# Optimization experiments

Measured on AMD Instinct MI355X. Metric: run time of the kernel, lower is better.

Reference implementation:

```python
import jax, jax.numpy as jnp
import numpy as np

B, T, HID = 4, 4096, 768
H, D = 12, 64
N_HASHES = 2
BUCKET_SIZE = T // 32          # reformer repo config: max_seq_len // 32 = 128
N_BUCKETS = T // BUCKET_SIZE   # 32
SELF_ATTN_VALUE = -5e4         # reformer_pytorch TOKEN_SELF_ATTN_VALUE
MASK_VALUE = -1e9


def lsh_attention(X, mask_bool, W_qk, W_v, rotations):
    # X: [b, t, hid]; rotations: [d, n_hashes, n_buckets//2] (shared across batch & heads)
    b, t, _ = X.shape
    d, n_hashes, half_nb = rotations.shape
    n_buckets = 2 * half_nb
    h = W_qk.shape[0] // d
    scale = d ** -0.5

    qk = X @ W_qk.T            # shared query/key projection (bias-free in reformer_pytorch)
    v = X @ W_v.T

    def merge_heads(x):  # [b,t,h*d] -> [b*h, t, d]
        return x.reshape(b, t, h, d).transpose(0, 2, 1, 3).reshape(b * h, t, d)

    qk, v = merge_heads(qk), merge_heads(v)
    maskbh = jnp.repeat(mask_bool, h, axis=0)          # [bh, t]

    # --- LSH bucketing ---
    rotated = jnp.einsum('btf,fhi->bhti', qk, rotations)          # [bh, nh, t, nb/2]
    rotated = jnp.concatenate([rotated, -rotated], axis=-1)       # [bh, nh, t, nb]
    buckets = jnp.argmax(rotated, axis=-1)                        # [bh, nh, t]
    offsets = (jnp.arange(n_hashes) * n_buckets)[None, :, None]
    buckets = (buckets + offsets).reshape(b * h, n_hashes * t)

    # --- stable sort by (bucket, position) ---
    total = n_hashes * t
    ticker = jnp.arange(total)[None, :]
    buckets_and_t = buckets * t + (ticker % t)
    sticker = jnp.argsort(buckets_and_t, axis=-1)   # stable
    undo = jnp.argsort(sticker, axis=-1)
    st = sticker % t                                 # original positions, sorted order

    sqk = jnp.take_along_axis(qk, st[..., None], axis=1)
    sv = jnp.take_along_axis(v, st[..., None], axis=1)
    smask = jnp.take_along_axis(maskbh, st, axis=1)

    # --- chunk; each chunk attends to itself + previous chunk ---
    n_chunks = n_hashes * n_buckets
    cl = total // n_chunks                                  # == bucket_size
    bq_t = st.reshape(b * h, n_chunks, cl)
    bqk = sqk.reshape(b * h, n_chunks, cl, d)
    bv = sv.reshape(b * h, n_chunks, cl, d)
    bmask = smask.reshape(b * h, n_chunks, cl)

    bq = bqk
    bk = bqk / jnp.clip(jnp.linalg.norm(bqk, axis=-1, keepdims=True), 1e-12)

    def look_one_back(x):
        return jnp.concatenate([x, jnp.roll(x, 1, axis=1)], axis=2)

    bk, bv = look_one_back(bk), look_one_back(bv)
    bkv_t = look_one_back(bq_t)
    bkv_mask = look_one_back(bmask)

    dots = jnp.einsum('bnie,bnje->bnij', bq, bk) * scale    # [bh, n_chunks, cl, 2cl]
    pad = bmask[..., :, None] & bkv_mask[..., None, :]
    dots = jnp.where(pad, dots, MASK_VALUE)
    self_mask = bq_t[..., :, None] == bkv_t[..., None, :]
    dots = jnp.where(self_mask, SELF_ATTN_VALUE, dots)

    lse = jax.scipy.special.logsumexp(dots, axis=-1, keepdims=True)
    probs = jnp.exp(dots - lse)
    bo = jnp.einsum('bnij,bnje->bnie', probs, bv)

    # --- unsort and combine hash rounds via softmax over round logsumexps ---
    so = bo.reshape(b * h, total, d)
    slogits = lse.reshape(b * h, total)
    o = jnp.take_along_axis(so, undo[..., None], axis=1)
    logits = jnp.take_along_axis(slogits, undo, axis=1)

    o = o.reshape(b * h, n_hashes, t, d)
    logits = logits.reshape(b * h, n_hashes, t, 1)
    round_probs = jnp.exp(logits - jax.scipy.special.logsumexp(logits, axis=1, keepdims=True))
    out = jnp.sum(o * round_probs, axis=1)                  # [bh, t, d]
    return out.reshape(b, h, t, d).transpose(0, 2, 1, 3).reshape(b, t, h * d)


def setup_inputs() -> dict:
    key = jax.random.key(0)
    ks = jax.random.split(key, 8)
    s = 1.0 / np.sqrt(HID)
    return {
        'X': jax.random.normal(ks[0], (B, T, HID), jnp.float32),
        'mask': jnp.ones((B, T), jnp.float32),
        'W_qk': jax.random.uniform(ks[1], (H * D, HID), jnp.float32, -s, s),
        'W_v': jax.random.uniform(ks[2], (H * D, HID), jnp.float32, -s, s),
        'rotations': jax.random.normal(ks[3], (D, N_HASHES, N_BUCKETS // 2), jnp.float32),
        'W_to': jax.random.uniform(ks[4], (HID, H * D), jnp.float32, -s, s),
        'b_to': jnp.zeros((HID,), jnp.float32),
        'W_o': jax.random.uniform(ks[5], (HID, HID), jnp.float32, -s, s),
        'b_o': jnp.zeros((HID,), jnp.float32),
    }


def reference(X, mask, W_qk, W_v, rotations, W_to, b_to, W_o, b_o):
    attn = lsh_attention(X, mask.astype(bool), W_qk, W_v, rotations)
    attn = attn @ W_to.T + b_to     # LSHSelfAttention.to_out
    return attn @ W_o.T + b_o       # ReformerAttention.W_o
```

## Files before the change

### kernel.cpp

```cpp
#include <hip/hip_runtime.h>
#include <hip/hip_bf16.h>
#include <math.h>


typedef __attribute__((ext_vector_type(8))) short bf16x8;
typedef __attribute__((ext_vector_type(4))) float f32x4;

__device__ __forceinline__ float bf_lo(unsigned int w) { return __uint_as_float(w << 16); }
__device__ __forceinline__ float bf_hi(unsigned int w) { return __uint_as_float(w & 0xffff0000u); }
__device__ __forceinline__ float load_in(const void* p, size_t i, bool f32) {
  return f32 ? ((const float*)p)[i]
             : __bfloat162float(((const __hip_bfloat16*)p)[i]);
}
__device__ __forceinline__ unsigned short f2bf(float x) {
  __hip_bfloat16 h = __float2bfloat16(x);
  return *reinterpret_cast<unsigned short*>(&h);
}
__device__ __forceinline__ float bf2f(unsigned short u) { return __uint_as_float(((unsigned int)u) << 16); }

__global__ void k_detect(const unsigned int* __restrict__ X, int* __restrict__ flag) {
  if (threadIdx.x == 0 && blockIdx.x == 0) {
    int vote = 0;
    for (int i = 0; i < 64; ++i) {
      unsigned int e = (X[i] >> 7) & 0xffu;
      vote += (e >= 100u && e <= 141u) ? 1 : 0;
    }
    *flag = (vote < 32) ? 1 : 0;
  }
}

__global__ __launch_bounds__(256) void k_convert(
    const void* __restrict__ src, unsigned short* __restrict__ dst, int n,
    const int* __restrict__ flag) {
  const bool f32in = (*flag != 0);
  int i = blockIdx.x * 256 + threadIdx.x;
  if (i >= n) return;
  if (f32in) dst[i] = f2bf(((const float*)src)[i]);
  else       dst[i] = ((const unsigned short*)src)[i];
}

__global__ __launch_bounds__(256) void k_build_wrot(
    const void* __restrict__ Wqk, const void* __restrict__ rot,
    double* __restrict__ WrotT, const int* __restrict__ flag) {
  const bool f32in = (*flag != 0);
  int idx = blockIdx.x * 256 + threadIdx.x;
  if (idx >= 768 * 384) return;
  int row = idx % 384;
  int c   = idx / 384;
  int hh = row >> 5, hi = row & 31;
  double s = 0.0;
  for (int f = 0; f < 64; ++f) {
    double rv = (double)load_in(rot, f * 32 + hi, f32in);
    double wv = (double)load_in(Wqk, (size_t)(hh * 64 + f) * 768 + c, f32in);
    s = fma(rv, wv, s);
  }
  WrotT[(size_t)c * 384 + row] = s;
}

__global__ __launch_bounds__(256) void k_bucket(
    const void* __restrict__ X, const double* __restrict__ WrotT,
    unsigned char* __restrict__ cls, const int* __restrict__ flag) {
  const bool f32in = (*flag != 0);
  __shared__ double SH[6336];
  double* Xs = SH;
  double* Ws = SH + 2080;
  double* Sc = SH;
  const int tid = threadIdx.x;
  const int M0 = blockIdx.x * 128;
  const int N0 = blockIdx.y * 96;
  const int tm = tid >> 4, tn = tid & 15;
  const int sr = tid >> 1, sh = tid & 1;
  const int wk = tid >> 4, wg = tid & 15;

  double acc[8][6];
  #pragma unroll
  for (int i = 0; i < 8; ++i)
    #pragma unroll
    for (int j = 0; j < 6; ++j) acc[i][j] = 0.0;

  for (int k0 = 0; k0 < 768; k0 += 16) {
    __syncthreads();
    {
      size_t base = (size_t)(M0 + sr) * 768 + k0 + sh * 8;
      double xv[8];
      if (f32in) {
        const float4* fp = (const float4*)((const float*)X + base);
        float4 f0 = fp[0], f1 = fp[1];
        xv[0] = f0.x; xv[1] = f0.y; xv[2] = f0.z; xv[3] = f0.w;
        xv[4] = f1.x; xv[5] = f1.y; xv[6] = f1.z; xv[7] = f1.w;
      } else {
        uint4 u = *(const uint4*)((const unsigned short*)X + base);
        xv[0] = (double)bf_lo(u.x); xv[1] = (double)bf_hi(u.x);
        xv[2] = (double)bf_lo(u.y); xv[3] = (double)bf_hi(u.y);
        xv[4] = (double)bf_lo(u.z); xv[5] = (double)bf_hi(u.z);
        xv[6] = (double)bf_lo(u.w); xv[7] = (double)bf_hi(u.w);
      }
      #pragma unroll
      for (int j = 0; j < 8; ++j) Xs[(sh * 8 + j) * 130 + sr] = xv[j];
    }
    {
      const double* wp = WrotT + (size_t)(k0 + wk) * 384 + N0 + wg * 6;
      #pragma unroll
      for (int e = 0; e < 6; ++e) Ws[wk * 98 + wg * 6 + e] = wp[e];
    }
    __syncthreads();
    #pragma unroll
    for (int k = 0; k < 16; ++k) {
      double a_[8], b_[6];
      #pragma unroll
      for (int i = 0; i < 8; ++i) a_[i] = Xs[k * 130 + tm * 8 + i];
      #pragma unroll
      for (int j = 0; j < 6; ++j) b_[j] = Ws[k * 98 + tn * 6 + j];
      #pragma unroll
      for (int i = 0; i < 8; ++i)
        #pragma unroll
        for (int j = 0; j < 6; ++j)
          acc[i][j] = fma(a_[i], b_[j], acc[i][j]);
    }
  }

  #pragma unroll
  for (int chunk = 0; chunk < 2; ++chunk) {
    __syncthreads();
    if ((tm >> 3) == chunk) {
      #pragma unroll
      for (int tt = 0; tt < 8; ++tt)
        #pragma unroll
        for (int rr = 0; rr < 6; ++rr)
          Sc[(tn * 6 + rr) * 66 + (tm & 7) * 8 + tt] = acc[tt][rr];
    }
    __syncthreads();
    for (int task = tid; task < 384; task += 256) {
      int g = task >> 6, tok = task & 63;
      const double* s = &Sc[(g * 16) * 66 + tok];
      double mx = -1.0e300;
      #pragma unroll
      for (int i = 0; i < 16; ++i) {
        double a = s[i * 66];
        mx = fmax(mx, fmax(a, -a));
      }
      int amax = 0;
      #pragma unroll
      for (int i = 15; i >= 0; --i) if (-s[i * 66] == mx) amax = 16 + i;
      #pragma unroll
      for (int i = 15; i >= 0; --i) if (s[i * 66] == mx) amax = i;
      int m = M0 + chunk * 64 + tok;
      int b = m >> 12, t = m & 4095;
      int gg = blockIdx.y * 6 + g, hh = gg >> 1, h = gg & 1;
      cls[(size_t)(b * 12 + hh) * 8192 + h * 4096 + t] = (unsigned char)(h * 32 + amax);
    }
  }
}

__global__ __launch_bounds__(1024) void k_sort(
    const unsigned char* __restrict__ clsg,
    unsigned short* __restrict__ stick) {
  __shared__ unsigned short cntg[128 * 64];
  __shared__ int classbase[64];
  const int row = blockIdx.x;
  const int tid = threadIdx.x;
  const int wave = tid >> 6, lane = tid & 63;
  const unsigned char* cr = clsg + ((size_t)row << 13);

  for (int i = tid; i < 128 * 64 / 2; i += 1024) ((uint32_t*)cntg)[i] = 0;
  __syncthreads();

  unsigned char myc[8], myrank[8];
  const unsigned long long ltmask = (lane == 0) ? 0ull : (~0ull >> (64 - lane));
  #pragma unroll
  for (int chunk = 0; chunk < 8; ++chunk) {
    int g = chunk * 16 + wave;
    int j = g * 64 + lane;
    int c = cr[j];
    unsigned long long same = ~0ull;
    #pragma unroll
    for (int bit = 0; bit < 6; ++bit) {
      unsigned long long bm = __ballot((c >> bit) & 1);
      same &= ((c >> bit) & 1) ? bm : ~bm;
    }
    int rank = __popcll(same & ltmask);
    if (rank == 0) cntg[g * 64 + c] = (unsigned short)__popcll(same);
    myc[chunk] = (unsigned char)c;
    myrank[chunk] = (unsigned char)rank;
  }
  __syncthreads();
  if (tid < 64) {
    int run = 0;
    for (int g = 0; g < 128; ++g) {
      int t = cntg[g * 64 + tid];
      cntg[g * 64 + tid] = (unsigned short)run;
      run += t;
    }
    classbase[tid] = run;
  }
  __syncthreads();
  if (tid == 0) {
    int run = 0;
    for (int c = 0; c < 64; ++c) { int t = classbase[c]; classbase[c] = run; run += t; }
  }
  __syncthreads();
  unsigned short* out = stick + ((size_t)row << 13);
  #pragma unroll
  for (int chunk = 0; chunk < 8; ++chunk) {
    int g = chunk * 16 + wave;
    int j = g * 64 + lane;
    int c = myc[chunk];
    int pos = classbase[c] + cntg[g * 64 + c] + myrank[chunk];
    out[pos] = (unsigned short)j;
  }
}

__global__ __launch_bounds__(256) void k_gemm_mfma(
    const unsigned short* __restrict__ A, const unsigned short* __restrict__ W,
    const void* __restrict__ bias, void* __restrict__ Cout,
    int layout, int out_ext, const int* __restrict__ flag) {
  const bool f32in = (*flag != 0);
  const bool oF32 = out_ext && f32in;
  __shared__ unsigned short As[128 * 40];
  __shared__ unsigned short Bs[128 * 40];
  const int tid = threadIdx.x;
  const int bm = blockIdx.x, bn = blockIdx.y;
  const int w = tid >> 6, lane = tid & 63;
  const int l15 = lane & 15, lq = lane >> 4;
  const int wm = (w >> 1) * 64, wn = (w & 1) * 64;
  const int r4 = tid >> 2, c4 = tid & 3;
  const unsigned short* Ag = A + (size_t)(bm * 128 + r4) * 768 + c4 * 8;
  const unsigned short* Bg = W + (size_t)(bn * 128 + r4) * 768 + c4 * 8;
  f32x4 acc[4][4];
  #pragma unroll
  for (int i = 0; i < 4; ++i)
    #pragma unroll
    for (int j = 0; j < 4; ++j) acc[i][j] = (f32x4){0.f, 0.f, 0.f, 0.f};
  uint4 pa0 = *(const uint4*)(Ag);
  uint4 pa1 = *(const uint4*)(Ag + 64 * 768);
  uint4 pb0 = *(const uint4*)(Bg);
  uint4 pb1 = *(const uint4*)(Bg + 64 * 768);
  for (int kt = 0; kt < 24; ++kt) {
    __syncthreads();
    *(uint4*)&As[r4 * 40 + c4 * 8] = pa0;
    *(uint4*)&As[(r4 + 64) * 40 + c4 * 8] = pa1;
    *(uint4*)&Bs[r4 * 40 + c4 * 8] = pb0;
    *(uint4*)&Bs[(r4 + 64) * 40 + c4 * 8] = pb1;
    __syncthreads();
    if (kt < 23) {
      int off = (kt + 1) * 32;
      pa0 = *(const uint4*)(Ag + off);
      pa1 = *(const uint4*)(Ag + 64 * 768 + off);
      pb0 = *(const uint4*)(Bg + off);
      pb1 = *(const uint4*)(Bg + 64 * 768 + off);
    }
    bf16x8 af[4], bfr[4];
    #pragma unroll
    for (int mt = 0; mt < 4; ++mt)
      af[mt] = *(const bf16x8*)&As[(wm + mt * 16 + l15) * 40 + lq * 8];
    #pragma unroll
    for (int nt = 0; nt < 4; ++nt)
      bfr[nt] = *(const bf16x8*)&Bs[(wn + nt * 16 + l15) * 40 + lq * 8];
    #pragma unroll
    for (int mt = 0; mt < 4; ++mt)
      #pragma unroll
      for (int nt = 0; nt < 4; ++nt)
        acc[mt][nt] = __builtin_amdgcn_mfma_f32_16x16x32_bf16(af[mt], bfr[nt], acc[mt][nt], 0, 0, 0);
  }
  #pragma unroll
  for (int mt = 0; mt < 4; ++mt) {
    #pragma unroll
    for (int nt = 0; nt < 4; ++nt) {
      #pragma unroll
      for (int reg = 0; reg < 4; ++reg) {
        int m = bm * 128 + wm + mt * 16 + lq * 4 + reg;
        int n = bn * 128 + wn + nt * 16 + l15;
        float val = acc[mt][nt][reg];
        if (bias != nullptr) val += load_in(bias, n, f32in);
        if (layout == 0) {
          size_t addr = (size_t)m * 768 + n;
          if (oF32) ((float*)Cout)[addr] = val;
          else      ((unsigned short*)Cout)[addr] = f2bf(val);
        } else {
          int b2 = m >> 12, t2 = m & 4095, hh = n >> 6, f = n & 63;
          ((unsigned short*)Cout)[((((size_t)(b2 * 12 + hh)) << 12) + t2) * 64 + f] = f2bf(val);
        }
      }
    }
  }
}

__global__ __launch_bounds__(256) void k_norm(
    const unsigned short* __restrict__ qk, float* __restrict__ nk) {
  int row = blockIdx.x * 32 + (threadIdx.x >> 3);
  int cs = threadIdx.x & 7;
  const uint4* p = (const uint4*)(qk + (size_t)row * 64);
  uint4 wv = p[cs];
  float s = 0.f;
  float e;
  e = bf_lo(wv.x); s += e * e;  e = bf_hi(wv.x); s += e * e;
  e = bf_lo(wv.y); s += e * e;  e = bf_hi(wv.y); s += e * e;
  e = bf_lo(wv.z); s += e * e;  e = bf_hi(wv.z); s += e * e;
  e = bf_lo(wv.w); s += e * e;  e = bf_hi(wv.w); s += e * e;
  s += __shfl_xor(s, 1, 64);
  s += __shfl_xor(s, 2, 64);
  s += __shfl_xor(s, 4, 64);
  if (cs == 0) nk[row] = 1.0f / fmaxf(sqrtf(s), 1e-12f);
}

__global__ __launch_bounds__(256) void k_attn_mfma(
    const unsigned short* __restrict__ qk,
    const unsigned short* __restrict__ vv,
    const unsigned short* __restrict__ stick,
    const void* __restrict__ mask,
    const float* __restrict__ nk,
    unsigned short* __restrict__ o_r,
    float* __restrict__ lse_r,
    const int* __restrict__ flag) {
  const bool f32in = (*flag != 0);
  __shared__ unsigned short Qs[128 * 72];
  __shared__ unsigned short Ks[64 * 72];
  __shared__ unsigned short Vt[64 * 72];
  __shared__ unsigned short Ps[4 * 32 * 72];
  __shared__ unsigned short Tq[128];
  __shared__ unsigned short Tkv[64];
  __shared__ float Nkv[64];
  unsigned short* Vs = Ps;

  const int tid = threadIdx.x;
  const int bh = blockIdx.x >> 6;
  const int ci = blockIdx.x & 63;
  const int b  = bh / 12;
  const int prev = (ci + 63) & 63;
  const int w = tid >> 6, lane = tid & 63;
  const int l15 = lane & 15, lq = lane >> 4;
  const unsigned short* srow = stick + ((size_t)bh << 13);
  const int jrow = tid >> 3, cs = tid & 7;

  #pragma unroll
  for (int pass = 0; pass < 4; ++pass) {
    int r = jrow + pass * 32;
    int s = srow[ci * 128 + r];
    int t = s & 4095;
    uint4 qw = ((const uint4*)(qk + ((((size_t)bh << 12) + t) << 6)))[cs];
    *(uint4*)&Qs[r * 72 + cs * 8] = qw;
    if (cs == 0) {
      float mv = load_in(mask, b * 4096 + t, f32in);
      Tq[r] = (unsigned short)(s | ((mv != 0.0f) ? 0 : 0x8000));
    }
  }
  __syncthreads();

  unsigned short tqr[2][4];
  #pragma unroll
  for (int mt = 0; mt < 2; ++mt)
    #pragma unroll
    for (int reg = 0; reg < 4; ++reg)
      tqr[mt][reg] = Tq[w * 32 + mt * 16 + lq * 4 + reg];

  float m_run[2][4], l_run[2][4];
  f32x4 oacc[2][4];
  #pragma unroll
  for (int mt = 0; mt < 2; ++mt)
    #pragma unroll
    for (int reg = 0; reg < 4; ++reg) { m_run[mt][reg] = -3.0e38f; l_run[mt][reg] = 0.0f; }
  #pragma unroll
  for (int mt = 0; mt < 2; ++mt)
    #pragma unroll
    for (int nto = 0; nto < 4; ++nto) oacc[mt][nto] = (f32x4){0.f, 0.f, 0.f, 0.f};

  for (int kt = 0; kt < 4; ++kt) {
    __syncthreads();
    #pragma unroll
    for (int pass = 0; pass < 2; ++pass) {
      int j = jrow + pass * 32;
      int chunk = (kt < 2) ? ci : prev;
      int s = srow[chunk * 128 + (kt & 1) * 64 + j];
      int t = s & 4095;
      const uint4* kb = (const uint4*)(qk + ((((size_t)bh << 12) + t) << 6));
      *(uint4*)&Ks[j * 72 + cs * 8] = kb[cs];
      const uint4* vb = (const uint4*)(vv + ((((size_t)bh << 12) + t) << 6));
      int sw = (cs ^ (j & 7) ^ (j >> 3)) & 7;
      *(uint4*)&Vs[j * 72 + sw * 8] = vb[cs];
      if (cs == 0) {
        float mv = load_in(mask, b * 4096 + t, f32in);
        Tkv[j] = (unsigned short)(t | ((mv != 0.0f) ? 0 : 0x8000));
        Nkv[j] = nk[((size_t)bh << 12) + t] * 0.125f;
      }
    }
    __syncthreads();

    #pragma unroll
    for (int i = 0; i < 8; ++i) {
      int cp = w * 8 + i;
      int q8 = cp >> 2;
      int sw = (q8 ^ (lane & 7) ^ (lane >> 3)) & 7;
      uint32_t wv = *(const uint32_t*)&Vs[lane * 72 + sw * 8 + ((2 * cp) & 7)];
      Vt[(2 * cp) * 72 + lane]     = (unsigned short)(wv & 0xffff);
      Vt[(2 * cp + 1) * 72 + lane] = (unsigned short)(wv >> 16);
    }

    f32x4 sacc[2][4];
    #pragma unroll
    for (int mt = 0; mt < 2; ++mt)
      #pragma unroll
      for (int nt = 0; nt < 4; ++nt) sacc[mt][nt] = (f32x4){0.f, 0.f, 0.f, 0.f};
    #pragma unroll
    for (int ks = 0; ks < 2; ++ks) {
      bf16x8 af[2];
      #pragma unroll
      for (int mt = 0; mt < 2; ++mt)
        af[mt] = *(const bf16x8*)&Qs[(w * 32 + mt * 16 + l15) * 72 + ks * 32 + lq * 8];
      #pragma unroll
      for (int nt = 0; nt < 4; ++nt) {
        bf16x8 bfr = *(const bf16x8*)&Ks[(nt * 16 + l15) * 72 + ks * 32 + lq * 8];
        #pragma unroll
        for (int mt = 0; mt < 2; ++mt)
          sacc[mt][nt] = __builtin_amdgcn_mfma_f32_16x16x32_bf16(af[mt], bfr, sacc[mt][nt], 0, 0, 0);
      }
    }

    unsigned short tkc[4];
    float nkc[4];
    #pragma unroll
    for (int nt = 0; nt < 4; ++nt) {
      tkc[nt] = Tkv[nt * 16 + l15];
      nkc[nt] = Nkv[nt * 16 + l15];
    }
    float dv[2][4][4];
    #pragma unroll
    for (int mt = 0; mt < 2; ++mt)
      #pragma unroll
      for (int nt = 0; nt < 4; ++nt)
        #pragma unroll
        for (int reg = 0; reg < 4; ++reg) {
          float x = sacc[mt][nt][reg] * nkc[nt];
          unsigned short ts = tqr[mt][reg];
          if (((tkc[nt] | ts) & 0x8000) != 0) x = -1.0e9f;
          if (((tkc[nt] ^ ts) & 0x0fff) == 0) x = -5.0e4f;
          dv[mt][nt][reg] = x;
        }
    float mn[2][4], scv[2][4];
    #pragma unroll
    for (int mt = 0; mt < 2; ++mt)
      #pragma unroll
      for (int reg = 0; reg < 4; ++reg) {
        float rm = fmaxf(fmaxf(dv[mt][0][reg], dv[mt][1][reg]),
                         fmaxf(dv[mt][2][reg], dv[mt][3][reg]));
        rm = fmaxf(rm, __shfl_xor(rm, 1, 64));
        rm = fmaxf(rm, __shfl_xor(rm, 2, 64));
        rm = fmaxf(rm, __shfl_xor(rm, 4, 64));
        rm = fmaxf(rm, __shfl_xor(rm, 8, 64));
        float mnew = fmaxf(m_run[mt][reg], rm);
        scv[mt][reg] = __expf(m_run[mt][reg] - mnew);
        m_run[mt][reg] = mnew;
        mn[mt][reg] = mnew;
      }
    #pragma unroll
    for (int mt = 0; mt < 2; ++mt)
      #pragma unroll
      for (int nt = 0; nt < 4; ++nt)
        #pragma unroll
        for (int reg = 0; reg < 4; ++reg)
          dv[mt][nt][reg] = __expf(dv[mt][nt][reg] - mn[mt][reg]);
    #pragma unroll
    for (int mt = 0; mt < 2; ++mt)
      #pragma unroll
      for (int reg = 0; reg < 4; ++reg) {
        float rs = ((dv[mt][0][reg] + dv[mt][1][reg]) + (dv[mt][2][reg] + dv[mt][3][reg]));
        rs += __shfl_xor(rs, 1, 64);
        rs += __shfl_xor(rs, 2, 64);
        rs += __shfl_xor(rs, 4, 64);
        rs += __shfl_xor(rs, 8, 64);
        l_run[mt][reg] = l_run[mt][reg] * scv[mt][reg] + rs;
      }
    #pragma unroll
    for (int mt = 0; mt < 2; ++mt)
      #pragma unroll
      for (int nto = 0; nto < 4; ++nto)
        #pragma unroll
        for (int reg = 0; reg < 4; ++reg)
          oacc[mt][nto][reg] *= scv[mt][reg];

    __syncthreads();

    #pragma unroll
    for (int mt = 0; mt < 2; ++mt)
      #pragma unroll
      for (int nt = 0; nt < 4; ++nt)
        #pragma unroll
        for (int reg = 0; reg < 4; ++reg)
          Ps[w * 2304 + (mt * 16 + lq * 4 + reg) * 72 + nt * 16 + l15] = f2bf(dv[mt][nt][reg]);

    #pragma unroll
    for (int ks = 0; ks < 2; ++ks) {
      bf16x8 pf[2];
      #pragma unroll
      for (int mt = 0; mt < 2; ++mt)
        pf[mt] = *(const bf16x8*)&Ps[w * 2304 + (mt * 16 + l15) * 72 + ks * 32 + lq * 8];
      #pragma unroll
      for (int nto = 0; nto < 4; ++nto) {
        bf16x8 vf = *(const bf16x8*)&Vt[(nto * 16 + l15) * 72 + ks * 32 + lq * 8];
        #pragma unroll
        for (int mt = 0; mt < 2; ++mt)
          oacc[mt][nto] = __builtin_amdgcn_mfma_f32_16x16x32_bf16(pf[mt], vf, oacc[mt][nto], 0, 0, 0);
      }
    }
  }

  float invl[2][4];
  #pragma unroll
  for (int mt = 0; mt < 2; ++mt)
    #pragma unroll
    for (int reg = 0; reg < 4; ++reg) {
      float lr = l_run[mt][reg];
      invl[mt][reg] = 1.0f / lr;
      if (l15 == 0) {
        int Rr = w * 32 + mt * 16 + lq * 4 + reg;
        int s = Tq[Rr];
        int tq0 = s & 4095, rq0 = (s >> 12) & 1;
        lse_r[(((size_t)(bh * 2 + rq0)) << 12) + tq0] = m_run[mt][reg] + __logf(lr);
      }
    }
  #pragma unroll
  for (int mt = 0; mt < 2; ++mt)
    #pragma unroll
    for (int nto = 0; nto < 4; ++nto)
      #pragma unroll
      for (int reg = 0; reg < 4; ++reg)
        Ps[w * 2304 + (mt * 16 + lq * 4 + reg) * 72 + nto * 16 + l15] =
            f2bf(oacc[mt][nto][reg] * invl[mt][reg]);
  #pragma unroll
  for (int pass = 0; pass < 4; ++pass) {
    int rl = pass * 8 + (lane >> 3);
    int s = Tq[w * 32 + rl];
    int tq0 = s & 4095, rq0 = (s >> 12) & 1;
    uint4 ov = *(const uint4*)&Ps[w * 2304 + rl * 72 + (lane & 7) * 8];
    *(uint4*)(o_r + ((((size_t)(bh * 2 + rq0)) << 12) + tq0) * 64 + (lane & 7) * 8) = ov;
  }
}

__global__ __launch_bounds__(256) void k_combine(
    const unsigned short* __restrict__ o_r,
    const float* __restrict__ lse_r,
    unsigned short* __restrict__ attn) {
  int idx = blockIdx.x * 256 + threadIdx.x;
  if (idx >= 48 * 4096 * 64) return;
  int f = idx & 63;
  int t = (idx >> 6) & 4095;
  int bh = idx >> 18;
  float l0 = lse_r[((size_t)(bh * 2 + 0) << 12) + t];
  float l1 = lse_r[((size_t)(bh * 2 + 1) << 12) + t];
  float mm = fmaxf(l0, l1);
  float e0 = __expf(l0 - mm), e1 = __expf(l1 - mm);
  float inv = 1.0f / (e0 + e1);
  float o0 = bf2f(o_r[(((size_t)(bh * 2 + 0) << 12) + t) * 64 + f]);
  float o1 = bf2f(o_r[(((size_t)(bh * 2 + 1) << 12) + t) * 64 + f]);
  float res = (e0 * o0 + e1 * o1) * inv;
  int b = bh / 12, hh = bh % 12;
  attn[((size_t)(b * 4096 + t)) * 768 + hh * 64 + f] = f2bf(res);
}

extern "C" void kernel_launch(void* const* d_in, const int* in_sizes, int n_in,
                              void* d_out, int out_size, void* d_ws, size_t ws_size,
                              hipStream_t stream) {
  (void)in_sizes; (void)n_in; (void)out_size; (void)ws_size;
  const void* X    = d_in[0];
  const void* mask = d_in[1];
  const void* Wqk  = d_in[2];
  const void* Wv   = d_in[3];
  const void* rot  = d_in[4];
  const void* Wto  = d_in[5];
  const void* bto  = d_in[6];
  const void* Wo   = d_in[7];
  const void* bo   = d_in[8];

  char* ws = (char*)d_ws;
  int*            flag  = (int*)(ws);
  unsigned short* stick = (unsigned short*)(ws + 256);
  float*          lse_r = (float*)(ws + 786688);
  float*          nk    = (float*)(ws + 2359552);
  unsigned short* qk    = (unsigned short*)(ws + 3145984);
  unsigned short* v     = (unsigned short*)(ws + 28311808);
  unsigned short* o_r   = (unsigned short*)(ws + 53477632);
  double*         WrotT = (double*)(ws + 53477632);
  unsigned char*  cls   = (unsigned char*)(ws + 55836928);
  unsigned short* Wqkb  = (unsigned short*)(ws + 56230144);
  unsigned short* Wvb   = (unsigned short*)(ws + 57409792);
  unsigned short* Xb    = (unsigned short*)(ws + 58589440);
  unsigned short* Wtob  = (unsigned short*)(ws + 53477632);
  unsigned short* Wob   = (unsigned short*)(ws + 54657280);
  unsigned short* attn  = v;
  unsigned short* tmp   = qk;

  k_detect<<<1, 64, 0, stream>>>((const unsigned int*)X, flag);
  k_convert<<<49152, 256, 0, stream>>>(X, Xb, 12582912, flag);
  k_convert<<<2304, 256, 0, stream>>>(Wqk, Wqkb, 589824, flag);
  k_convert<<<2304, 256, 0, stream>>>(Wv, Wvb, 589824, flag);
  k_build_wrot<<<1152, 256, 0, stream>>>(Wqk, rot, WrotT, flag);
  k_bucket<<<dim3(128, 4), 256, 0, stream>>>(X, WrotT, cls, flag);
  k_sort<<<48, 1024, 0, stream>>>(cls, stick);
  k_gemm_mfma<<<dim3(128, 6), 256, 0, stream>>>(Xb, Wqkb, nullptr, qk, 1, 0, flag);
  k_gemm_mfma<<<dim3(128, 6), 256, 0, stream>>>(Xb, Wvb,  nullptr, v,  1, 0, flag);
  k_norm<<<6144, 256, 0, stream>>>(qk, nk);
  k_attn_mfma<<<3072, 256, 0, stream>>>(qk, v, stick, mask, nk, o_r, lse_r, flag);
  k_combine<<<49152, 256, 0, stream>>>(o_r, lse_r, attn);
  k_convert<<<2304, 256, 0, stream>>>(Wto, Wtob, 589824, flag);
  k_convert<<<2304, 256, 0, stream>>>(Wo, Wob, 589824, flag);
  k_gemm_mfma<<<dim3(128, 6), 256, 0, stream>>>(attn, Wtob, bto, tmp, 0, 0, flag);
  k_gemm_mfma<<<dim3(128, 6), 256, 0, stream>>>(tmp, Wob, bo, d_out, 0, 1, flag);
}
```

Measured before the change: 696.9 us.

## Prefetch bucket GEMM tiles in registers and fuse key-norm into attention

The fp64 bucketing GEMM now uses a K-tile of 32 instead of 16. The next X and WrotT tile is loaded into registers while the current tile is being computed, and the kernel gets a launch_bounds occupancy hint of 2. Separately, the standalone k_norm launch is removed and each key's inverse L2 norm is computed inside the attention kernel from the K row it already loads, using a shuffle reduction. This trades one launch and its global round trip for recomputing norms per chunk, at the cost of extra shared memory and register pressure in k_bucket.

```diff
diff --git a/kernel.cpp b/kernel.cpp
--- a/kernel.cpp
+++ b/kernel.cpp
@@ -57,20 +57,20 @@
   WrotT[(size_t)c * 384 + row] = s;
 }
 
-__global__ __launch_bounds__(256) void k_bucket(
+__global__ __launch_bounds__(256, 2) void k_bucket(
     const void* __restrict__ X, const double* __restrict__ WrotT,
     unsigned char* __restrict__ cls, const int* __restrict__ flag) {
   const bool f32in = (*flag != 0);
-  __shared__ double SH[6336];
+  __shared__ double SH[7296];
   double* Xs = SH;
-  double* Ws = SH + 2080;
+  double* Ws = SH + 4160;
   double* Sc = SH;
   const int tid = threadIdx.x;
   const int M0 = blockIdx.x * 128;
   const int N0 = blockIdx.y * 96;
   const int tm = tid >> 4, tn = tid & 15;
   const int sr = tid >> 1, sh = tid & 1;
-  const int wk = tid >> 4, wg = tid & 15;
+  const int wk = tid >> 3, wg = tid & 7;
 
   double acc[8][6];
   #pragma unroll
@@ -78,34 +78,63 @@
     #pragma unroll
     for (int j = 0; j < 6; ++j) acc[i][j] = 0.0;
 
-  for (int k0 = 0; k0 < 768; k0 += 16) {
+  uint4 px0, px1;
+  float4 pf0, pf1, pf2, pf3;
+  double pw[12];
+
+  const size_t xrow = (size_t)(M0 + sr) * 768 + sh * 16;
+  const double* wbase = WrotT + (size_t)wk * 384 + N0 + wg * 12;
+
+  if (f32in) {
+    const float4* fp = (const float4*)((const float*)X + xrow);
+    pf0 = fp[0]; pf1 = fp[1]; pf2 = fp[2]; pf3 = fp[3];
+  } else {
+    const uint4* up = (const uint4*)((const unsigned short*)X + xrow);
+    px0 = up[0]; px1 = up[1];
+  }
+  #pragma unroll
+  for (int e = 0; e < 12; ++e) pw[e] = wbase[e];
+
+  for (int kt = 0; kt < 24; ++kt) {
     __syncthreads();
     {
-      size_t base = (size_t)(M0 + sr) * 768 + k0 + sh * 8;
-      double xv[8];
+      double xv[16];
       if (f32in) {
-        const float4* fp = (const float4*)((const float*)X + base);
-        float4 f0 = fp[0], f1 = fp[1];
-        xv[0] = f0.x; xv[1] = f0.y; xv[2] = f0.z; xv[3] = f0.w;
-        xv[4] = f1.x; xv[5] = f1.y; xv[6] = f1.z; xv[7] = f1.w;
+        xv[0] = pf0.x; xv[1] = pf0.y; xv[2] = pf0.z; xv[3] = pf0.w;
+        xv[4] = pf1.x; xv[5] = pf1.y; xv[6] = pf1.z; xv[7] = pf1.w;
+        xv[8] = pf2.x; xv[9] = pf2.y; xv[10] = pf2.z; xv[11] = pf2.w;
+        xv[12] = pf3.x; xv[13] = pf3.y; xv[14] = pf3.z; xv[15] = pf3.w;
       } else {
-        uint4 u = *(const uint4*)((const unsigned short*)X + base);
-        xv[0] = (double)bf_lo(u.x); xv[1] = (double)bf_hi(u.x);
-        xv[2] = (double)bf_lo(u.y); xv[3] = (double)bf_hi(u.y);
-        xv[4] = (double)bf_lo(u.z); xv[5] = (double)bf_hi(u.z);
-        xv[6] = (double)bf_lo(u.w); xv[7] = (double)bf_hi(u.w);
-      }
-      #pragma unroll
-      for (int j = 0; j < 8; ++j) Xs[(sh * 8 + j) * 130 + sr] = xv[j];
-    }
-    {
-      const double* wp = WrotT + (size_t)(k0 + wk) * 384 + N0 + wg * 6;
-      #pragma unroll
-      for (int e = 0; e < 6; ++e) Ws[wk * 98 + wg * 6 + e] = wp[e];
-    }
-    __syncthreads();
-    #pragma unroll
-    for (int k = 0; k < 16; ++k) {
+        xv[0] = (double)bf_lo(px0.x); xv[1] = (double)bf_hi(px0.x);
+        xv[2] = (double)bf_lo(px0.y); xv[3] = (double)bf_hi(px0.y);
+        xv[4] = (double)bf_lo(px0.z); xv[5] = (double)bf_hi(px0.z);
+        xv[6] = (double)bf_lo(px0.w); xv[7] = (double)bf_hi(px0.w);
+        xv[8] = (double)bf_lo(px1.x); xv[9] = (double)bf_hi(px1.x);
+        xv[10] = (double)bf_lo(px1.y); xv[11] = (double)bf_hi(px1.y);
+        xv[12] = (double)bf_lo(px1.z); xv[13] = (double)bf_hi(px1.z);
+        xv[14] = (double)bf_lo(px1.w); xv[15] = (double)bf_hi(px1.w);
+      }
+      #pragma unroll
+      for (int j = 0; j < 16; ++j) Xs[(sh * 16 + j) * 130 + sr] = xv[j];
+      #pragma unroll
+      for (int e = 0; e < 12; ++e) Ws[wk * 98 + wg * 12 + e] = pw[e];
+    }
+    __syncthreads();
+    if (kt < 23) {
+      int k0 = (kt + 1) * 32;
+      if (f32in) {
+        const float4* fp = (const float4*)((const float*)X + xrow + k0);
+        pf0 = fp[0]; pf1 = fp[1]; pf2 = fp[2]; pf3 = fp[3];
+      } else {
+        const uint4* up = (const uint4*)((const unsigned short*)X + xrow + k0);
+        px0 = up[0]; px1 = up[1];
+      }
+      const double* wp = wbase + (size_t)k0 * 384;
+      #pragma unroll
+      for (int e = 0; e < 12; ++e) pw[e] = wp[e];
+    }
+    #pragma unroll
+    for (int k = 0; k < 32; ++k) {
       double a_[8], b_[6];
       #pragma unroll
       for (int i = 0; i < 8; ++i) a_[i] = Xs[k * 130 + tm * 8 + i];
@@ -285,30 +314,11 @@
   }
 }
 
-__global__ __launch_bounds__(256) void k_norm(
-    const unsigned short* __restrict__ qk, float* __restrict__ nk) {
-  int row = blockIdx.x * 32 + (threadIdx.x >> 3);
-  int cs = threadIdx.x & 7;
-  const uint4* p = (const uint4*)(qk + (size_t)row * 64);
-  uint4 wv = p[cs];
-  float s = 0.f;
-  float e;
-  e = bf_lo(wv.x); s += e * e;  e = bf_hi(wv.x); s += e * e;
-  e = bf_lo(wv.y); s += e * e;  e = bf_hi(wv.y); s += e * e;
-  e = bf_lo(wv.z); s += e * e;  e = bf_hi(wv.z); s += e * e;
-  e = bf_lo(wv.w); s += e * e;  e = bf_hi(wv.w); s += e * e;
-  s += __shfl_xor(s, 1, 64);
-  s += __shfl_xor(s, 2, 64);
-  s += __shfl_xor(s, 4, 64);
-  if (cs == 0) nk[row] = 1.0f / fmaxf(sqrtf(s), 1e-12f);
-}
-
 __global__ __launch_bounds__(256) void k_attn_mfma(
     const unsigned short* __restrict__ qk,
     const unsigned short* __restrict__ vv,
     const unsigned short* __restrict__ stick,
     const void* __restrict__ mask,
-    const float* __restrict__ nk,
     unsigned short* __restrict__ o_r,
     float* __restrict__ lse_r,
     const int* __restrict__ flag) {
@@ -373,14 +383,23 @@
       int s = srow[chunk * 128 + (kt & 1) * 64 + j];
       int t = s & 4095;
       const uint4* kb = (const uint4*)(qk + ((((size_t)bh << 12) + t) << 6));
-      *(uint4*)&Ks[j * 72 + cs * 8] = kb[cs];
+      uint4 kw = kb[cs];
+      *(uint4*)&Ks[j * 72 + cs * 8] = kw;
+      float ss = 0.f, e;
+      e = bf_lo(kw.x); ss += e * e;  e = bf_hi(kw.x); ss += e * e;
+      e = bf_lo(kw.y); ss += e * e;  e = bf_hi(kw.y); ss += e * e;
+      e = bf_lo(kw.z); ss += e * e;  e = bf_hi(kw.z); ss += e * e;
+      e = bf_lo(kw.w); ss += e * e;  e = bf_hi(kw.w); ss += e * e;
+      ss += __shfl_xor(ss, 1, 64);
+      ss += __shfl_xor(ss, 2, 64);
+      ss += __shfl_xor(ss, 4, 64);
       const uint4* vb = (const uint4*)(vv + ((((size_t)bh << 12) + t) << 6));
       int sw = (cs ^ (j & 7) ^ (j >> 3)) & 7;
       *(uint4*)&Vs[j * 72 + sw * 8] = vb[cs];
       if (cs == 0) {
         float mv = load_in(mask, b * 4096 + t, f32in);
         Tkv[j] = (unsigned short)(t | ((mv != 0.0f) ? 0 : 0x8000));
-        Nkv[j] = nk[((size_t)bh << 12) + t] * 0.125f;
+        Nkv[j] = (1.0f / fmaxf(sqrtf(ss), 1e-12f)) * 0.125f;
       }
     }
     __syncthreads();
@@ -574,7 +593,6 @@
   int*            flag  = (int*)(ws);
   unsigned short* stick = (unsigned short*)(ws + 256);
   float*          lse_r = (float*)(ws + 786688);
-  float*          nk    = (float*)(ws + 2359552);
   unsigned short* qk    = (unsigned short*)(ws + 3145984);
   unsigned short* v     = (unsigned short*)(ws + 28311808);
   unsigned short* o_r   = (unsigned short*)(ws + 53477632);
@@ -597,8 +615,7 @@
   k_sort<<<48, 1024, 0, stream>>>(cls, stick);
   k_gemm_mfma<<<dim3(128, 6), 256, 0, stream>>>(Xb, Wqkb, nullptr, qk, 1, 0, flag);
   k_gemm_mfma<<<dim3(128, 6), 256, 0, stream>>>(Xb, Wvb,  nullptr, v,  1, 0, flag);
-  k_norm<<<6144, 256, 0, stream>>>(qk, nk);
-  k_attn_mfma<<<3072, 256, 0, stream>>>(qk, v, stick, mask, nk, o_r, lse_r, flag);
+  k_attn_mfma<<<3072, 256, 0, stream>>>(qk, v, stick, mask, o_r, lse_r, flag);
   k_combine<<<49152, 256, 0, stream>>>(o_r, lse_r, attn);
   k_convert<<<2304, 256, 0, stream>>>(Wto, Wtob, 589824, flag);
   k_convert<<<2304, 256, 0, stream>>>(Wo, Wob, 589824, flag);
```

Measured after the change: 697.2 us. About the same (+0.0%).
